# Optimization experiments

Measured on AMD Instinct MI355X. Metric: run time of the kernel, lower is better.

## Reference

```python
import jax, jax.numpy as jnp
import numpy as np

B, T, H = 1, 1024, 2048
HK, HV, DK, DV, K = 8, 16, 128, 128, 4
KD = HK * DK          # 1024
VD = HV * DV          # 2048
CD = 2 * KD + VD      # conv channels: q|k|v = 4096
EPS = 1e-6


def setup_inputs() -> dict:
    key = jax.random.key(0)
    ks = jax.random.split(key, 9)
    sc = lambda k, shape, s=0.02: jax.random.normal(k, shape, jnp.float32) * s
    return {
        "x": jax.random.normal(ks[0], (B, T, H), jnp.float32),
        "w_qkvz": sc(ks[1], (H, 2 * KD + 2 * VD)),
        "w_ba": sc(ks[2], (H, 2 * HV)),
        "conv_w": sc(ks[3], (CD, K), 0.2),
        "conv_b": jnp.zeros((CD,), jnp.float32),
        "a_log": jnp.log(jax.random.uniform(ks[4], (HV,), jnp.float32, 0.5, 4.0)),
        "dt_bias": sc(ks[5], (HV,), 0.5),
        "norm_w": jnp.ones((DV,), jnp.float32),
        "w_o": sc(ks[6], (VD, H)),
    }


def _l2norm(t):
    return t * jax.lax.rsqrt(jnp.sum(t * t, axis=-1, keepdims=True) + EPS)


def _gdn_forward(x, w_qkvz, w_ba, conv_w, conv_b, a_log, dt_bias, norm_w, w_o):
    # fused qkvz projection  [B,T, 2*KD + 2*VD]
    qkvz = x @ w_qkvz
    q, k, v, z = jnp.split(qkvz, [KD, 2 * KD, 2 * KD + VD], axis=-1)
    ba = x @ w_ba
    b, a = jnp.split(ba, [HV], axis=-1)  # [B,T,HV] each

    # causal depthwise conv1d over time on concatenated q|k|v channels, then SiLU
    mixed = jnp.concatenate([q, k, v], axis=-1)          # [B,T,CD]
    xc = jnp.moveaxis(mixed, 1, 2)                       # [B,CD,T]
    xc = jnp.pad(xc, ((0, 0), (0, 0), (K - 1, 0)))       # left pad -> causal
    yc = jax.lax.conv_general_dilated(
        xc, conv_w[:, None, :], (1,), "VALID",
        dimension_numbers=("NCH", "OIH", "NCH"), feature_group_count=CD)
    yc = jax.nn.silu(yc + conv_b[None, :, None])
    mixed = jnp.moveaxis(yc, 1, 2)                       # [B,T,CD]
    q, k, v = jnp.split(mixed, [KD, 2 * KD], axis=-1)

    q = q.reshape(B, T, HK, DK)
    k = k.reshape(B, T, HK, DK)
    v = v.reshape(B, T, HV, DV)

    # qk l2 norm (use_qk_l2norm_in_kernel) + GQA repeat + scale
    q = _l2norm(q)
    k = _l2norm(k)
    groups = HV // HK
    q = jnp.repeat(q, groups, axis=2)                    # [B,T,HV,DK]
    k = jnp.repeat(k, groups, axis=2)
    q = q * (DK ** -0.5)

    beta = jax.nn.sigmoid(b)                                        # [B,T,HV]
    g = -jnp.exp(a_log)[None, None, :] * jax.nn.softplus(a + dt_bias[None, None, :])

    # gated delta rule recurrence over time
    def step(S, inp):
        qt, kt, vt, gt, bt = inp                         # [B,HV,*]
        S = S * jnp.exp(gt)[..., None, None]             # decay
        pred = jnp.einsum("bhk,bhkv->bhv", kt, S)        # retrieve
        delta = (vt - pred) * bt[..., None]              # delta update
        S = S + kt[..., None] * delta[:, :, None, :]
        o = jnp.einsum("bhk,bhkv->bhv", qt, S)
        return S, o

    S0 = jnp.zeros((B, HV, DK, DV), jnp.float32)
    xs = tuple(jnp.moveaxis(t, 1, 0) for t in (q, k, v, g, beta))
    _, o = jax.lax.scan(step, S0, xs)                    # o: [T,B,HV,DV]
    o = jnp.moveaxis(o, 0, 1)                            # [B,T,HV,DV]

    # gated RMSNorm: gate first (silu), then normalize, then scale
    zg = z.reshape(B, T, HV, DV)
    h = o * jax.nn.silu(zg)
    h = h * jax.lax.rsqrt(jnp.mean(h * h, axis=-1, keepdims=True) + EPS)
    h = h * norm_w

    return h.reshape(B, T, VD) @ w_o                     # [B,T,H]


def reference(x, w_qkvz, w_ba, conv_w, conv_b, a_log, dt_bias, norm_w, w_o):
    return _gdn_forward(x, w_qkvz, w_ba, conv_w, conv_b, a_log, dt_bias, norm_w, w_o)
```

## Files before the change

### kernel.cpp

```cpp
#include <hip/hip_runtime.h>
#include <math.h>

typedef unsigned short u16;
using us4  = __attribute__((ext_vector_type(4))) unsigned short;
using us8  = __attribute__((ext_vector_type(8))) unsigned short;
using bf16x8 = __attribute__((ext_vector_type(8))) __bf16;
using f32x4v = __attribute__((ext_vector_type(4))) float;

#define T_    1024
#define H_    2048
#define HK_   8
#define HV_   16
#define KD_   1024
#define VD_   2048
#define CD_   4096
#define QN_   6144
#define NC_   16
#define C_    64

__device__ __forceinline__ u16 f2bf(float f) {
  unsigned u = __float_as_uint(f);
  u += 0x7fffu + ((u >> 16) & 1u);
  return (u16)(u >> 16);
}
__device__ __forceinline__ float bf2f(u16 h) {
  return __uint_as_float(((unsigned)h) << 16);
}
__device__ __forceinline__ int permk3(int r, int k) {
  return (k & ~63) | ((((k >> 3) & 7) ^ (r & 7)) << 3) | (k & 7);
}

__global__ void cast_bf16(const float* __restrict__ in, u16* __restrict__ out,
                          int n8) {
  int i = blockIdx.x * 256 + threadIdx.x;
  if (i >= n8) return;
  float4 a = ((const float4*)in)[i * 2];
  float4 b = ((const float4*)in)[i * 2 + 1];
  us8 r = {f2bf(a.x), f2bf(a.y), f2bf(a.z), f2bf(a.w),
           f2bf(b.x), f2bf(b.y), f2bf(b.z), f2bf(b.w)};
  const int row = i >> 8;
  const int ip = (i & ~7) | ((i & 7) ^ (row & 7));
  *(us8*)&out[(size_t)ip * 8] = r;
}

__global__ __launch_bounds__(256) void transpose_bf16(
    const float* __restrict__ in, u16* __restrict__ out, int R, int C) {
  __shared__ float tile[64][65];
  const int r0 = blockIdx.x * 64, c0 = blockIdx.y * 64;
  const int t = threadIdx.x;
  const int tr = t >> 4, tc4 = (t & 15) * 4;
#pragma unroll
  for (int i = 0; i < 4; ++i) {
    float4 v = *(const float4*)&in[(size_t)(r0 + tr + i * 16) * C + c0 + tc4];
    tile[tr + i * 16][tc4 + 0] = v.x;
    tile[tr + i * 16][tc4 + 1] = v.y;
    tile[tr + i * 16][tc4 + 2] = v.z;
    tile[tr + i * 16][tc4 + 3] = v.w;
  }
  __syncthreads();
#pragma unroll
  for (int i = 0; i < 4; ++i) {
    int oc = tr + i * 16;
    int row = c0 + oc;
    int k = r0 + tc4;
    us4 w = {f2bf(tile[tc4 + 0][oc]), f2bf(tile[tc4 + 1][oc]),
             f2bf(tile[tc4 + 2][oc]), f2bf(tile[tc4 + 3][oc])};
    *(us4*)&out[(size_t)row * R + permk3(row, k)] = w;
  }
}

__device__ __forceinline__ void gload_lds16(const void* g, void* l) {
  __builtin_amdgcn_global_load_lds(
      (const __attribute__((address_space(1))) void*)g,
      (__attribute__((address_space(3))) void*)l, 16, 0, 0);
}

__global__ __launch_bounds__(256) void gemm_bf16(
    const u16* __restrict__ A, const u16* __restrict__ Bt,
    float* __restrict__ Cq, int ldq, float* __restrict__ Cz, int ldz,
    int zsplit, int M, int N, int K) {
  __shared__ __align__(16) u16 As[2][8192];
  __shared__ __align__(16) u16 Bs[2][4096];
  const int tid  = threadIdx.x;
  const int wave = tid >> 6, lane = tid & 63;
  const int gy = N >> 6;
  const int ncolpx = gy >> 3;
  const int bid = blockIdx.x;
  const int xcd = bid & 7, idx = bid >> 3;
  const int row0 = (idx / ncolpx) * 128;
  const int col0 = (xcd * ncolpx + idx % ncolpx) * 64;
  const int wr = wave >> 1, wc = wave & 1;
  const int fr = lane & 15, fq = lane >> 4;

  const int sr8 = lane >> 3;
  const int sc8 = (lane & 7) * 8;
  const u16* gA = A  + (size_t)(row0 + wave * 32 + sr8) * K + sc8;
  const u16* gB = Bt + (size_t)(col0 + wave * 16 + sr8) * K + sc8;

  f32x4v acc[4][2] = {};
  const int nt = K >> 6;

  auto stage = [&](int p, int k0) {
#pragma unroll
    for (int j = 0; j < 4; ++j)
      gload_lds16(gA + (size_t)(j * 8) * K + k0,
                  &As[p][(wave * 32 + j * 8) * 64]);
#pragma unroll
    for (int j = 0; j < 2; ++j)
      gload_lds16(gB + (size_t)(j * 8) * K + k0,
                  &Bs[p][(wave * 16 + j * 8) * 64]);
  };

  stage(0, 0);
  asm volatile("s_waitcnt vmcnt(0)" ::: "memory");
  __syncthreads();

  int p = 0;
  for (int it = 0; it < nt; ++it) {
    if (it + 1 < nt) stage(p ^ 1, (it + 1) * 64);
#pragma unroll
    for (int kt = 0; kt < 2; ++kt) {
      bf16x8 af[4], bff[2];
#pragma unroll
      for (int mi = 0; mi < 4; ++mi) {
        const int r = wr * 64 + mi * 16 + fr;
        af[mi] = *(const bf16x8*)
            &As[p][r * 64 + kt * 32 + (((kt * 4 + fq) ^ (r & 7)) & 3) * 8
                   + ((((kt * 4 + fq) ^ (r & 7)) >> 2) - kt) * 32];
      }
#pragma unroll
      for (int ni = 0; ni < 2; ++ni) {
        const int r = wc * 32 + ni * 16 + fr;
        bff[ni] = *(const bf16x8*)
            &Bs[p][r * 64 + kt * 32 + (((kt * 4 + fq) ^ (r & 7)) & 3) * 8
                   + ((((kt * 4 + fq) ^ (r & 7)) >> 2) - kt) * 32];
      }
#pragma unroll
      for (int mi = 0; mi < 4; ++mi)
#pragma unroll
        for (int ni = 0; ni < 2; ++ni)
          acc[mi][ni] = __builtin_amdgcn_mfma_f32_16x16x32_bf16(
              af[mi], bff[ni], acc[mi][ni], 0, 0, 0);
    }
    if (it + 1 < nt) {
      asm volatile("s_waitcnt vmcnt(0)" ::: "memory");
      __syncthreads();
    }
    p ^= 1;
  }

  float* Cp; int ldc, cb;
  if (col0 < zsplit) { Cp = Cq; ldc = ldq; cb = col0; }
  else               { Cp = Cz; ldc = ldz; cb = col0 - zsplit; }
#pragma unroll
  for (int mi = 0; mi < 4; ++mi)
#pragma unroll
    for (int ni = 0; ni < 2; ++ni) {
      const int r  = row0 + wr * 64 + mi * 16 + fq * 4;
      const int cc = cb + wc * 32 + ni * 16 + fr;
#pragma unroll
      for (int j = 0; j < 4; ++j)
        Cp[(size_t)(r + j) * ldc + cc] = acc[mi][ni][j];
    }
}

__global__ __launch_bounds__(256) void ba_gbeta(
    const float* __restrict__ x, const float* __restrict__ w_ba,
    const float* __restrict__ a_log, const float* __restrict__ dt_bias,
    float* __restrict__ g, float* __restrict__ beta) {
  const int t = blockIdx.x;
  const int tid = threadIdx.x;
  __shared__ float xs[2048];
  __shared__ float red[8][32];
  {
    float4 v = *(const float4*)&x[(size_t)t * H_ + tid * 4];
    *(float4*)&xs[tid * 4] = v;
    float4 w = *(const float4*)&x[(size_t)t * H_ + 1024 + tid * 4];
    *(float4*)&xs[1024 + tid * 4] = w;
  }
  __syncthreads();
  const int c = tid & 31;
  const int chunk = tid >> 5;
  float p = 0.f;
  const int kb = chunk * 256;
#pragma unroll 4
  for (int k = kb; k < kb + 256; ++k) p = fmaf(xs[k], w_ba[k * 32 + c], p);
  red[chunk][c] = p;
  __syncthreads();
  if (tid < 32) {
    float s = 0.f;
#pragma unroll
    for (int i = 0; i < 8; ++i) s += red[i][c];
    if (c < 16) {
      beta[t * 16 + c] = 1.f / (1.f + expf(-s));
    } else {
      int h = c - 16;
      float xx = s + dt_bias[h];
      float sp = xx > 20.f ? xx : log1pf(expf(xx));
      g[t * 16 + h] = -expf(a_log[h]) * sp;
    }
  }
}

__global__ __launch_bounds__(512) void conv_silu_k(
    const float* __restrict__ qkvraw, const float* __restrict__ conv_w,
    const float* __restrict__ conv_b, float* __restrict__ qkvc,
    float* __restrict__ khat) {
  const int t = blockIdx.x;
  const int tid = threadIdx.x;
  const int c0 = tid * 8;
  float acc[8];
  float4 cb0 = *(const float4*)&conv_b[c0];
  float4 cb1 = *(const float4*)&conv_b[c0 + 4];
  acc[0] = cb0.x; acc[1] = cb0.y; acc[2] = cb0.z; acc[3] = cb0.w;
  acc[4] = cb1.x; acc[5] = cb1.y; acc[6] = cb1.z; acc[7] = cb1.w;
  float wv[8][4];
#pragma unroll
  for (int i = 0; i < 8; i += 2) {
    float4 w0 = *(const float4*)&conv_w[(c0 + i) * 4];
    float4 w1 = *(const float4*)&conv_w[(c0 + i + 1) * 4];
    wv[i][0] = w0.x; wv[i][1] = w0.y; wv[i][2] = w0.z; wv[i][3] = w0.w;
    wv[i+1][0] = w1.x; wv[i+1][1] = w1.y; wv[i+1][2] = w1.z; wv[i+1][3] = w1.w;
  }
#pragma unroll
  for (int j = 0; j < 4; ++j) {
    int tt = t - 3 + j;
    if (tt >= 0) {
      float4 a = *(const float4*)&qkvraw[(size_t)tt * CD_ + c0];
      float4 b = *(const float4*)&qkvraw[(size_t)tt * CD_ + c0 + 4];
      float xv[8] = {a.x, a.y, a.z, a.w, b.x, b.y, b.z, b.w};
#pragma unroll
      for (int i = 0; i < 8; ++i) acc[i] = fmaf(xv[i], wv[i][j], acc[i]);
    }
  }
  float y[8];
#pragma unroll
  for (int i = 0; i < 8; ++i) y[i] = acc[i] / (1.f + expf(-acc[i]));

  if (tid < 128 || tid >= 256) {
    float4 o0 = {y[0], y[1], y[2], y[3]};
    float4 o1 = {y[4], y[5], y[6], y[7]};
    *(float4*)&qkvc[(size_t)t * CD_ + c0]     = o0;
    *(float4*)&qkvc[(size_t)t * CD_ + c0 + 4] = o1;
  } else {
    float ss = 0.f;
#pragma unroll
    for (int i = 0; i < 8; ++i) ss = fmaf(y[i], y[i], ss);
#pragma unroll
    for (int off = 1; off < 16; off <<= 1) ss += __shfl_xor(ss, off);
    float rs = rsqrtf(ss + 1e-6f);
    const int head = (c0 - 1024) >> 7;
    const int d0 = (c0 - 1024) & 127;
    float4 o0 = {y[0] * rs, y[1] * rs, y[2] * rs, y[3] * rs};
    float4 o1 = {y[4] * rs, y[5] * rs, y[6] * rs, y[7] * rs};
    float* kout = &khat[((size_t)t * HK_ + head) * 128 + d0];
    *(float4*)&kout[0] = o0;
    *(float4*)&kout[4] = o1;
  }
}

#define SWZ(r) (((r) >> 2) & 7)

__device__ __forceinline__ float4 ldsw4(const float* base, int r, int dblk) {
  return *(const float4*)&base[r * 128 + ((dblk ^ SWZ(r)) << 2)];
}
__device__ __forceinline__ float ldsw1(const float* base, int r, int d) {
  return base[r * 128 + ((((d) >> 2) ^ SWZ(r)) << 2) + ((d) & 3)];
}

__global__ __launch_bounds__(512) void chunk_prep(
    const float* __restrict__ qkvc, const float* __restrict__ khat,
    const float* __restrict__ g, const float* __restrict__ beta,
    float* __restrict__ cgbuf, float* __restrict__ Wtg, float* __restrict__ Ug,
    float* __restrict__ Mqg, float* __restrict__ pQg) {
  const int c = blockIdx.x, hv = blockIdx.y, hk = hv >> 1;
  const int cid = c * 16 + hv;
  const int tid = threadIdx.x;
  __shared__ float Kl[8192], Ql[8192];
  __shared__ float AM[8320];
  __shared__ float cgl[64], bl[64], bp[64], rsl[64];
  float* At = AM;
  float* Mq = AM + 4160;

#pragma unroll
  for (int it = 0; it < 4; ++it) {
    int flat = it * 2048 + tid * 4;
    int row = flat >> 7, d = flat & 127;
    int pb = ((d >> 2) ^ SWZ(row)) << 2;
    int gt = c * 64 + row;
    float4 kv = *(const float4*)&khat[((size_t)gt * HK_ + hk) * 128 + d];
    float4 qv = *(const float4*)&qkvc[(size_t)gt * CD_ + hk * 128 + d];
    *(float4*)&Kl[row * 128 + pb] = kv;
    *(float4*)&Ql[row * 128 + pb] = qv;
  }
  if (tid < 64) {
    float s = g[(size_t)(c * 64 + tid) * HV_ + hv];
#pragma unroll
    for (int off = 1; off < 64; off <<= 1) {
      float t = __shfl_up(s, off);
      if (tid >= off) s += t;
    }
    cgl[tid] = s;
    cgbuf[cid * 64 + tid] = s;
    bl[tid] = beta[(size_t)(c * 64 + tid) * HV_ + hv];
  }
  __syncthreads();
  if (tid < 64) {
    float sq = 0.f;
#pragma unroll
    for (int dblk = 0; dblk < 32; ++dblk) {
      float4 q4 = ldsw4(Ql, tid, dblk);
      sq = fmaf(q4.x, q4.x, sq); sq = fmaf(q4.y, q4.y, sq);
      sq = fmaf(q4.z, q4.z, sq); sq = fmaf(q4.w, q4.w, sq);
    }
    rsl[tid] = rsqrtf(sq + 1e-6f) * 0.08838834764831845f;
    bp[tid] = bl[tid] * expf(cgl[tid]);
  }
  __syncthreads();

  const int i0 = (tid >> 5) * 4, j0 = (tid & 31) * 2;
  float kk[4][2], qk[4][2];
#pragma unroll
  for (int a = 0; a < 4; ++a)
#pragma unroll
    for (int b = 0; b < 2; ++b) { kk[a][b] = 0.f; qk[a][b] = 0.f; }
  for (int dblk = 0; dblk < 32; ++dblk) {
    float4 ka[4], qa[4], kb[2];
#pragma unroll
    for (int a = 0; a < 4; ++a) {
      ka[a] = ldsw4(Kl, i0 + a, dblk);
      qa[a] = ldsw4(Ql, i0 + a, dblk);
    }
#pragma unroll
    for (int b = 0; b < 2; ++b) kb[b] = ldsw4(Kl, j0 + b, dblk);
#pragma unroll
    for (int a = 0; a < 4; ++a)
#pragma unroll
      for (int b = 0; b < 2; ++b) {
        kk[a][b] = fmaf(ka[a].x, kb[b].x, kk[a][b]);
        kk[a][b] = fmaf(ka[a].y, kb[b].y, kk[a][b]);
        kk[a][b] = fmaf(ka[a].z, kb[b].z, kk[a][b]);
        kk[a][b] = fmaf(ka[a].w, kb[b].w, kk[a][b]);
        qk[a][b] = fmaf(qa[a].x, kb[b].x, qk[a][b]);
        qk[a][b] = fmaf(qa[a].y, kb[b].y, qk[a][b]);
        qk[a][b] = fmaf(qa[a].z, kb[b].z, qk[a][b]);
        qk[a][b] = fmaf(qa[a].w, kb[b].w, qk[a][b]);
      }
  }
#pragma unroll
  for (int a = 0; a < 4; ++a)
#pragma unroll
    for (int b = 0; b < 2; ++b) {
      int i = i0 + a, j = j0 + b;
      float e = expf(cgl[i] - cgl[j]);
      At[j * 65 + i] = (j < i) ? (-bl[i] * e * kk[a][b]) : 0.f;
      Mq[j * 65 + i] = (j <= i) ? (rsl[i] * e * qk[a][b]) : 0.f;
    }
  __syncthreads();

  float X[64];
  if (tid < 256) {
    if (tid < 128) {
#pragma unroll
      for (int j = 0; j < 64; ++j) X[j] = bp[j] * ldsw1(Kl, j, tid);
    } else {
      const int m = tid - 128;
#pragma unroll
      for (int j = 0; j < 64; ++j)
        X[j] = bl[j] * qkvc[(size_t)(c * 64 + j) * CD_ + 2 * KD_ + hv * 128 + m];
    }
#pragma unroll
    for (int j = 0; j < 63; ++j) {
      float xj = X[j];
#pragma unroll
      for (int i = j + 1; i < 64; ++i) X[i] = fmaf(At[j * 65 + i], xj, X[i]);
    }
    if (tid < 128) {
      size_t baseo = ((size_t)cid * 128 + tid) * 64;
#pragma unroll
      for (int j4 = 0; j4 < 16; ++j4) {
        float4 v = {X[j4 * 4], X[j4 * 4 + 1], X[j4 * 4 + 2], X[j4 * 4 + 3]};
        *(float4*)&Wtg[baseo + j4 * 4] = v;
      }
    }
  } else {
    const int t2 = tid - 256;
#pragma unroll
    for (int it = 0; it < 16; ++it) {
      int f = it * 256 + t2;
      int j = f >> 6, i = f & 63;
      Mqg[(size_t)cid * 4096 + f] = Mq[j * 65 + i];
    }
    const int i = t2 & 63;
    const float ei = expf(cgl[i]) * rsl[i];
#pragma unroll
    for (int it = 0; it < 32; ++it) {
      int d = it * 4 + (t2 >> 6);
      pQg[(size_t)cid * 8192 + d * 64 + i] = ei * ldsw1(Ql, i, d);
    }
  }
  __syncthreads();

  if (tid >= 128 && tid < 256) {
    const int m = tid - 128;
    float* Utr = AM;
#pragma unroll
    for (int j = 0; j < 64; ++j) Utr[j * 128 + m] = X[j];
  }
  __syncthreads();
  {
    const float* Utr = AM;
#pragma unroll
    for (int it = 0; it < 4; ++it) {
      int flat = it * 2048 + tid * 4;
      *(float4*)&Ug[(size_t)cid * 8192 + flat] = *(const float4*)&Utr[flat];
    }
  }
}

__global__ __launch_bounds__(512) void make_MBG(
    const float* __restrict__ Wtg, const float* __restrict__ pQg,
    const float* __restrict__ Ug, const float* __restrict__ Mqg,
    const float* __restrict__ khat, const float* __restrict__ cgbuf,
    u16* __restrict__ Mhi, u16* __restrict__ Mlo,
    float* __restrict__ Bg, float* __restrict__ Gtg) {
  const int c = blockIdx.x, hv = blockIdx.y, hk = hv >> 1;
  const int cid = c * 16 + hv;
  const int tid = threadIdx.x;
  __shared__ float Wl[64 * 128];
  __shared__ float Kel[64 * 128];
  __shared__ float Ul[64 * 128];
  __shared__ float Mql[64 * 64];
  const float cg63 = cgbuf[cid * 64 + 63];
  const float pC = expf(cg63);
#pragma unroll
  for (int it = 0; it < 4; ++it) {
    int f = it * 2048 + tid * 4;
    int d = f >> 6, j = f & 63;
    float4 w = *(const float4*)&Wtg[(size_t)cid * 8192 + f];
    Wl[(j + 0) * 128 + d] = w.x;
    Wl[(j + 1) * 128 + d] = w.y;
    Wl[(j + 2) * 128 + d] = w.z;
    Wl[(j + 3) * 128 + d] = w.w;
  }
#pragma unroll
  for (int it = 0; it < 4; ++it) {
    int f = it * 2048 + tid * 4;
    int j = f >> 7, d = f & 127;
    float esc = expf(cg63 - cgbuf[cid * 64 + j]);
    float4 kv = *(const float4*)&khat[((size_t)(c * 64 + j) * HK_ + hk) * 128 + d];
    float4 uv = *(const float4*)&Ug[(size_t)cid * 8192 + f];
    kv.x *= esc; kv.y *= esc; kv.z *= esc; kv.w *= esc;
    *(float4*)&Kel[f] = kv;
    *(float4*)&Ul[f] = uv;
  }
#pragma unroll
  for (int it = 0; it < 2; ++it) {
    int f = it * 2048 + tid * 4;
    *(float4*)&Mql[f] = *(const float4*)&Mqg[(size_t)cid * 4096 + f];
  }
  __syncthreads();

  const int d0 = (tid & 15) * 8, n0 = (tid >> 4) * 4;
  float ma[8][4] = {}, ba[8][4] = {};
  for (int j = 0; j < 64; ++j) {
    float4 k0 = *(const float4*)&Kel[j * 128 + d0];
    float4 k1 = *(const float4*)&Kel[j * 128 + d0 + 4];
    float4 w0 = *(const float4*)&Wl[j * 128 + n0];
    float4 u0 = *(const float4*)&Ul[j * 128 + n0];
    float ke[8] = {k0.x, k0.y, k0.z, k0.w, k1.x, k1.y, k1.z, k1.w};
    float wv[4] = {w0.x, w0.y, w0.z, w0.w};
    float uv[4] = {u0.x, u0.y, u0.z, u0.w};
#pragma unroll
    for (int a = 0; a < 8; ++a)
#pragma unroll
      for (int b = 0; b < 4; ++b) {
        ma[a][b] = fmaf(ke[a], wv[b], ma[a][b]);
        ba[a][b] = fmaf(ke[a], uv[b], ba[a][b]);
      }
  }
#pragma unroll
  for (int a = 0; a < 8; ++a) {
    const int d = d0 + a;
    us4 hi, lo;
#pragma unroll
    for (int b = 0; b < 4; ++b) {
      float m = ((d == n0 + b) ? pC : 0.f) - ma[a][b];
      u16 h = f2bf(m);
      hi[b] = h;
      lo[b] = f2bf(m - bf2f(h));
    }
    *(us4*)&Mhi[(size_t)cid * 16384 + d * 128 + n0] = hi;
    *(us4*)&Mlo[(size_t)cid * 16384 + d * 128 + n0] = lo;
    float4 b0 = {ba[a][0], ba[a][1], ba[a][2], ba[a][3]};
    *(float4*)&Bg[(size_t)cid * 16384 + d * 128 + n0] = b0;
  }

  const int dg = (tid & 31) * 4, ig = (tid >> 5) * 4;
  float ga[4][4] = {};
  for (int j = 0; j < 64; ++j) {
    float4 w4 = *(const float4*)&Wl[j * 128 + dg];
    float4 m0 = *(const float4*)&Mql[j * 64 + ig];
    float wv[4] = {w4.x, w4.y, w4.z, w4.w};
    float mv[4] = {m0.x, m0.y, m0.z, m0.w};
#pragma unroll
    for (int a = 0; a < 4; ++a)
#pragma unroll
      for (int b = 0; b < 4; ++b) ga[a][b] = fmaf(wv[a], mv[b], ga[a][b]);
  }
#pragma unroll
  for (int a = 0; a < 4; ++a) {
    const int d = dg + a;
    float4 p0 = *(const float4*)&pQg[(size_t)cid * 8192 + d * 64 + ig];
    float4 g0 = {p0.x - ga[a][0], p0.y - ga[a][1], p0.z - ga[a][2], p0.w - ga[a][3]};
    *(float4*)&Gtg[(size_t)cid * 8192 + d * 64 + ig] = g0;
  }
}

__global__ __launch_bounds__(512) void scan_S(
    const u16* __restrict__ Mhi, const u16* __restrict__ Mlo,
    const float* __restrict__ Bg, float* __restrict__ Sg) {
  const int flat = blockIdx.x;
  const int hv = (flat & 7) + 8 * (flat >> 6);
  const int vs = (flat >> 3) & 7;
  const int tid = threadIdx.x;
  const int wave = tid >> 6, lane = tid & 63;
  const int fr = lane & 15, fq = lane >> 4;
  const int wr = wave * 16;
  const int m0 = vs * 16;

  __shared__ u16 Sh[2][2048];
  __shared__ u16 Sl[2][2048];

  for (int i = tid; i < 2048; i += 512) { Sh[0][i] = 0; Sl[0][i] = 0; }
  {
    float* s0 = Sg + (size_t)hv * 16384 + m0;
#pragma unroll
    for (int it = 0; it < 4; ++it) {
      int idx = it * 512 + tid;
      s0[(size_t)(idx >> 4) * 128 + (idx & 15)] = 0.f;
    }
  }
  __syncthreads();

  bf16x8 MhA[4], MlA[4], MhB[4], MlB[4];
  float bvA[4], bvB[4];
  {
    const u16* Mh0 = Mhi + (size_t)hv * 16384;
    const u16* Ml0 = Mlo + (size_t)hv * 16384;
#pragma unroll
    for (int kt = 0; kt < 4; ++kt) {
      size_t off = (size_t)(wr + fr) * 128 + kt * 32 + fq * 8;
      MhA[kt] = *(const bf16x8*)&Mh0[off];
      MlA[kt] = *(const bf16x8*)&Ml0[off];
    }
    const float* Bc = Bg + (size_t)hv * 16384 + m0;
#pragma unroll
    for (int j = 0; j < 4; ++j)
      bvA[j] = Bc[(size_t)(wr + fq * 4 + j) * 128 + fr];
  }
  int p = 0;

  auto step = [&](int c, bf16x8 (&MhC)[4], bf16x8 (&MlC)[4], float (&bvC)[4],
                  bf16x8 (&MhN)[4], bf16x8 (&MlN)[4], float (&bvN)[4]) {
    if (c + 1 < NC_ - 1) {
      const u16* MhP = Mhi + (size_t)((c + 1) * 16 + hv) * 16384;
      const u16* MlP = Mlo + (size_t)((c + 1) * 16 + hv) * 16384;
#pragma unroll
      for (int kt = 0; kt < 4; ++kt) {
        size_t off = (size_t)(wr + fr) * 128 + kt * 32 + fq * 8;
        MhN[kt] = *(const bf16x8*)&MhP[off];
        MlN[kt] = *(const bf16x8*)&MlP[off];
      }
      const float* BcN = Bg + (size_t)((c + 1) * 16 + hv) * 16384 + m0;
#pragma unroll
      for (int j = 0; j < 4; ++j)
        bvN[j] = BcN[(size_t)(wr + fq * 4 + j) * 128 + fr];
    }

    f32x4v acc = {};
#pragma unroll
    for (int kt = 0; kt < 4; ++kt) {
      const int m = fr;
      const int byte = m * 256 + ((kt * 64 + fq * 16) ^ ((m & 7) << 4));
      bf16x8 BhF = *(const bf16x8*)((const char*)&Sh[p][0] + byte);
      bf16x8 BlF = *(const bf16x8*)((const char*)&Sl[p][0] + byte);
      acc = __builtin_amdgcn_mfma_f32_16x16x32_bf16(MlC[kt], BhF, acc, 0, 0, 0);
      acc = __builtin_amdgcn_mfma_f32_16x16x32_bf16(MhC[kt], BlF, acc, 0, 0, 0);
      acc = __builtin_amdgcn_mfma_f32_16x16x32_bf16(MhC[kt], BhF, acc, 0, 0, 0);
    }

    float* Sn = Sg + (size_t)((c + 1) * 16 + hv) * 16384 + m0;
    const int k0 = wr + fq * 4;
    const int m = fr;
    us4 h4, l4;
#pragma unroll
    for (int j = 0; j < 4; ++j) {
      float v = acc[j] + bvC[j];
      Sn[(size_t)(k0 + j) * 128 + m] = v;
      u16 h = f2bf(v);
      h4[j] = h;
      l4[j] = f2bf(v - bf2f(h));
    }
    const int wbyte = m * 256 + ((k0 * 2) ^ ((m & 7) << 4));
    *(us4*)((char*)&Sh[p ^ 1][0] + wbyte) = h4;
    *(us4*)((char*)&Sl[p ^ 1][0] + wbyte) = l4;
    __syncthreads();
    p ^= 1;
  };

  for (int cc = 0; cc < NC_ - 1; cc += 2) {
    step(cc, MhA, MlA, bvA, MhB, MlB, bvB);
    if (cc + 1 < NC_ - 1) step(cc + 1, MhB, MlB, bvB, MhA, MlA, bvA);
  }
}

__global__ __launch_bounds__(256) void chunk_out(
    const float* __restrict__ Mqg, const float* __restrict__ Ug,
    const float* __restrict__ Gtg, const float* __restrict__ Sg,
    float* __restrict__ o) {
  const int c = blockIdx.x, hv = blockIdx.y;
  const int cid = c * 16 + hv;
  const int tid = threadIdx.x;
  __shared__ float Mql[64 * 64];
  __shared__ float Ul[64 * 128];
  __shared__ float Gtl[128 * 64];
  __shared__ float Sl[128 * 128];
#pragma unroll
  for (int it = 0; it < 4; ++it) {
    int f = it * 1024 + tid * 4;
    *(float4*)&Mql[f] = *(const float4*)&Mqg[(size_t)cid * 4096 + f];
  }
#pragma unroll
  for (int it = 0; it < 8; ++it) {
    int f = it * 1024 + tid * 4;
    *(float4*)&Ul[f]  = *(const float4*)&Ug[(size_t)cid * 8192 + f];
    *(float4*)&Gtl[f] = *(const float4*)&Gtg[(size_t)cid * 8192 + f];
  }
#pragma unroll
  for (int it = 0; it < 16; ++it) {
    int f = it * 1024 + tid * 4;
    *(float4*)&Sl[f] = *(const float4*)&Sg[(size_t)cid * 16384 + f];
  }
  __syncthreads();

  const int i0 = (tid & 15) * 4, m0 = (tid >> 4) * 8;
  float oa[4][8] = {};
  for (int j = 0; j < 64; ++j) {
    float4 mq = *(const float4*)&Mql[j * 64 + i0];
    float4 u0 = *(const float4*)&Ul[j * 128 + m0];
    float4 u1 = *(const float4*)&Ul[j * 128 + m0 + 4];
    float mv[4] = {mq.x, mq.y, mq.z, mq.w};
    float uv[8] = {u0.x, u0.y, u0.z, u0.w, u1.x, u1.y, u1.z, u1.w};
#pragma unroll
    for (int a = 0; a < 4; ++a)
#pragma unroll
      for (int b = 0; b < 8; ++b) oa[a][b] = fmaf(mv[a], uv[b], oa[a][b]);
  }
  for (int d = 0; d < 128; ++d) {
    float4 gt = *(const float4*)&Gtl[d * 64 + i0];
    float4 s0 = *(const float4*)&Sl[d * 128 + m0];
    float4 s1 = *(const float4*)&Sl[d * 128 + m0 + 4];
    float gv[4] = {gt.x, gt.y, gt.z, gt.w};
    float sv[8] = {s0.x, s0.y, s0.z, s0.w, s1.x, s1.y, s1.z, s1.w};
#pragma unroll
    for (int a = 0; a < 4; ++a)
#pragma unroll
      for (int b = 0; b < 8; ++b) oa[a][b] = fmaf(gv[a], sv[b], oa[a][b]);
  }
#pragma unroll
  for (int a = 0; a < 4; ++a) {
    const int t = c * 64 + i0 + a;
    float4 o0 = {oa[a][0], oa[a][1], oa[a][2], oa[a][3]};
    float4 o1 = {oa[a][4], oa[a][5], oa[a][6], oa[a][7]};
    *(float4*)&o[((size_t)t * HV_ + hv) * 128 + m0]     = o0;
    *(float4*)&o[((size_t)t * HV_ + hv) * 128 + m0 + 4] = o1;
  }
}

__global__ void gated_rmsnorm(const float* __restrict__ o,
                              const float* __restrict__ zbuf,
                              const float* __restrict__ norm_w,
                              u16* __restrict__ h) {
  const int t = blockIdx.x, hv = blockIdx.y, d = threadIdx.x;
  float ov = o[((size_t)t * HV_ + hv) * 128 + d];
  float zv = zbuf[(size_t)t * VD_ + hv * 128 + d];
  float hc = ov * (zv / (1.f + expf(-zv)));
  float ss = hc * hc;
#pragma unroll
  for (int off = 32; off >= 1; off >>= 1) ss += __shfl_xor(ss, off);
  __shared__ float s2[2];
  if ((d & 63) == 0) s2[d >> 6] = ss;
  __syncthreads();
  float tot = s2[0] + s2[1];
  float r = rsqrtf(tot * (1.f / 128.f) + 1e-6f);
  const int k = hv * 128 + d;
  h[(size_t)t * VD_ + permk3(t, k)] = f2bf(hc * r * norm_w[d]);
}

extern "C" void kernel_launch(void* const* d_in, const int* in_sizes, int n_in,
                              void* d_out, int out_size, void* d_ws, size_t ws_size,
                              hipStream_t stream) {
  const float* x       = (const float*)d_in[0];
  const float* w_qkvz  = (const float*)d_in[1];
  const float* w_ba    = (const float*)d_in[2];
  const float* conv_w  = (const float*)d_in[3];
  const float* conv_b  = (const float*)d_in[4];
  const float* a_log   = (const float*)d_in[5];
  const float* dt_bias = (const float*)d_in[6];
  const float* norm_w  = (const float*)d_in[7];
  const float* w_o     = (const float*)d_in[8];
  float* out = (float*)d_out;

  float* ws = (float*)d_ws;
  float* qkvraw = ws;
  float* zbuf   = ws + 4194304;
  float* qkvc   = ws + 6291456;
  float* khat   = ws + 10485760;
  float* gbuf   = ws + 11534336;
  float* bbuf   = ws + 11550720;
  float* cgbuf  = ws + 11567104;
  float* obuf   = ws + 11583488;
  float* Wtg    = ws + 13680640;
  float* pQg    = ws + 15777792;
  float* Ug     = ws + 17874944;
  float* Mqg    = ws + 19972096;
  float* Gtg    = ws + 21020672;

  u16* xb   = (u16*)obuf;
  u16* wqt  = (u16*)Wtg;
  u16* Mhi  = (u16*)qkvc;
  u16* Mlo  = (u16*)(qkvc + 2097152);
  float* Bg = qkvraw;
  float* Sg = Wtg;
  u16* wot  = (u16*)qkvc;
  u16* hb   = (u16*)khat;

  cast_bf16<<<1024, 256, 0, stream>>>(x, xb, 262144);
  transpose_bf16<<<dim3(32, 96), 256, 0, stream>>>(w_qkvz, wqt, H_, QN_);
  gemm_bf16<<<768, 256, 0, stream>>>(xb, wqt, qkvraw, CD_, zbuf, VD_,
                                     CD_, T_, QN_, H_);
  ba_gbeta<<<T_, 256, 0, stream>>>(x, w_ba, a_log, dt_bias, gbuf, bbuf);
  conv_silu_k<<<T_, 512, 0, stream>>>(qkvraw, conv_w, conv_b, qkvc, khat);
  chunk_prep<<<dim3(NC_, HV_), 512, 0, stream>>>(
      qkvc, khat, gbuf, bbuf, cgbuf, Wtg, Ug, Mqg, pQg);
  make_MBG<<<dim3(NC_, HV_), 512, 0, stream>>>(
      Wtg, pQg, Ug, Mqg, khat, cgbuf, Mhi, Mlo, Bg, Gtg);
  scan_S<<<128, 512, 0, stream>>>(Mhi, Mlo, Bg, Sg);
  transpose_bf16<<<dim3(32, 32), 256, 0, stream>>>(w_o, wot, VD_, H_);
  chunk_out<<<dim3(NC_, HV_), 256, 0, stream>>>(Mqg, Ug, Gtg, Sg, obuf);
  gated_rmsnorm<<<dim3(T_, HV_), 128, 0, stream>>>(obuf, zbuf, norm_w, hb);
  gemm_bf16<<<256, 256, 0, stream>>>(hb, wot, out, VD_, out, VD_,
                                     VD_, T_, VD_, H_);
}
```

Before: 246.7 us.

## Compute chunk KK^T and QK^T with split-bf16 MFMA, vectorize triangular solve

The chunk_prep kernel now stores K and Q in shared memory as hi/lo bf16 pairs with an XOR swizzle. It computes the 64x64 K·K^T and Q·K^T products with three-term split-bf16 MFMA instructions instead of scalar FP32 FMAs. The At matrix stride is padded to 68 so the forward-substitution loop can read coefficients as float4. Shared memory use grows and the split-bf16 path is slightly less exact than FP32, but the work is moved onto matrix cores.

```diff
diff --git a/kernel.cpp b/kernel.cpp
--- a/kernel.cpp
+++ b/kernel.cpp
@@ -261,9 +261,6 @@
 
 #define SWZ(r) (((r) >> 2) & 7)
 
-__device__ __forceinline__ float4 ldsw4(const float* base, int r, int dblk) {
-  return *(const float4*)&base[r * 128 + ((dblk ^ SWZ(r)) << 2)];
-}
 __device__ __forceinline__ float ldsw1(const float* base, int r, int d) {
   return base[r * 128 + ((((d) >> 2) ^ SWZ(r)) << 2) + ((d) & 3)];
 }
@@ -276,22 +273,34 @@
   const int c = blockIdx.x, hv = blockIdx.y, hk = hv >> 1;
   const int cid = c * 16 + hv;
   const int tid = threadIdx.x;
-  __shared__ float Kl[8192], Ql[8192];
-  __shared__ float AM[8320];
+  __shared__ __align__(16) float Kl[8192];
+  __shared__ __align__(16) u16 KhiL[8192], KloL[8192];
+  __shared__ __align__(16) u16 QhiL[8192], QloL[8192];
+  __shared__ __align__(16) float AM[8512];
   __shared__ float cgl[64], bl[64], bp[64], rsl[64];
   float* At = AM;
-  float* Mq = AM + 4160;
+  float* Mq = AM + 4352;
 
 #pragma unroll
   for (int it = 0; it < 4; ++it) {
     int flat = it * 2048 + tid * 4;
     int row = flat >> 7, d = flat & 127;
-    int pb = ((d >> 2) ^ SWZ(row)) << 2;
     int gt = c * 64 + row;
     float4 kv = *(const float4*)&khat[((size_t)gt * HK_ + hk) * 128 + d];
     float4 qv = *(const float4*)&qkvc[(size_t)gt * CD_ + hk * 128 + d];
+    int pb = ((d >> 2) ^ SWZ(row)) << 2;
     *(float4*)&Kl[row * 128 + pb] = kv;
-    *(float4*)&Ql[row * 128 + pb] = qv;
+    int ba = row * 128 + (((d >> 3) ^ (row & 15)) << 3) + (d & 7);
+    us4 kh = {f2bf(kv.x), f2bf(kv.y), f2bf(kv.z), f2bf(kv.w)};
+    us4 kl = {f2bf(kv.x - bf2f(kh[0])), f2bf(kv.y - bf2f(kh[1])),
+              f2bf(kv.z - bf2f(kh[2])), f2bf(kv.w - bf2f(kh[3]))};
+    us4 qh = {f2bf(qv.x), f2bf(qv.y), f2bf(qv.z), f2bf(qv.w)};
+    us4 ql = {f2bf(qv.x - bf2f(qh[0])), f2bf(qv.y - bf2f(qh[1])),
+              f2bf(qv.z - bf2f(qh[2])), f2bf(qv.w - bf2f(qh[3]))};
+    *(us4*)&KhiL[ba] = kh;
+    *(us4*)&KloL[ba] = kl;
+    *(us4*)&QhiL[ba] = qh;
+    *(us4*)&QloL[ba] = ql;
   }
   if (tid < 64) {
     float s = g[(size_t)(c * 64 + tid) * HV_ + hv];
@@ -308,54 +317,63 @@
   if (tid < 64) {
     float sq = 0.f;
 #pragma unroll
-    for (int dblk = 0; dblk < 32; ++dblk) {
-      float4 q4 = ldsw4(Ql, tid, dblk);
-      sq = fmaf(q4.x, q4.x, sq); sq = fmaf(q4.y, q4.y, sq);
-      sq = fmaf(q4.z, q4.z, sq); sq = fmaf(q4.w, q4.w, sq);
+    for (int ch = 0; ch < 16; ++ch) {
+      int ba = tid * 128 + ((ch ^ (tid & 15)) << 3);
+      us8 h8 = *(const us8*)&QhiL[ba];
+      us8 l8 = *(const us8*)&QloL[ba];
+#pragma unroll
+      for (int e = 0; e < 8; ++e) {
+        float q = bf2f(h8[e]) + bf2f(l8[e]);
+        sq = fmaf(q, q, sq);
+      }
     }
     rsl[tid] = rsqrtf(sq + 1e-6f) * 0.08838834764831845f;
     bp[tid] = bl[tid] * expf(cgl[tid]);
   }
   __syncthreads();
 
-  const int i0 = (tid >> 5) * 4, j0 = (tid & 31) * 2;
-  float kk[4][2], qk[4][2];
-#pragma unroll
-  for (int a = 0; a < 4; ++a)
-#pragma unroll
-    for (int b = 0; b < 2; ++b) { kk[a][b] = 0.f; qk[a][b] = 0.f; }
-  for (int dblk = 0; dblk < 32; ++dblk) {
-    float4 ka[4], qa[4], kb[2];
-#pragma unroll
-    for (int a = 0; a < 4; ++a) {
-      ka[a] = ldsw4(Kl, i0 + a, dblk);
-      qa[a] = ldsw4(Ql, i0 + a, dblk);
-    }
-#pragma unroll
-    for (int b = 0; b < 2; ++b) kb[b] = ldsw4(Kl, j0 + b, dblk);
-#pragma unroll
-    for (int a = 0; a < 4; ++a)
-#pragma unroll
-      for (int b = 0; b < 2; ++b) {
-        kk[a][b] = fmaf(ka[a].x, kb[b].x, kk[a][b]);
-        kk[a][b] = fmaf(ka[a].y, kb[b].y, kk[a][b]);
-        kk[a][b] = fmaf(ka[a].z, kb[b].z, kk[a][b]);
-        kk[a][b] = fmaf(ka[a].w, kb[b].w, kk[a][b]);
-        qk[a][b] = fmaf(qa[a].x, kb[b].x, qk[a][b]);
-        qk[a][b] = fmaf(qa[a].y, kb[b].y, qk[a][b]);
-        qk[a][b] = fmaf(qa[a].z, kb[b].z, qk[a][b]);
-        qk[a][b] = fmaf(qa[a].w, kb[b].w, qk[a][b]);
-      }
-  }
-#pragma unroll
-  for (int a = 0; a < 4; ++a)
-#pragma unroll
-    for (int b = 0; b < 2; ++b) {
-      int i = i0 + a, j = j0 + b;
-      float e = expf(cgl[i] - cgl[j]);
-      At[j * 65 + i] = (j < i) ? (-bl[i] * e * kk[a][b]) : 0.f;
-      Mq[j * 65 + i] = (j <= i) ? (rsl[i] * e * qk[a][b]) : 0.f;
-    }
+  {
+    const int wv = tid >> 6, lane = tid & 63;
+    const int fr = lane & 15, fq = lane >> 4;
+    const int ib = wv & 3;
+    const int jb0 = (wv >> 2) * 2;
+    const int ra = ib * 16 + fr;
+    bf16x8 KhA[4], KlA[4], QhA[4], QlA[4];
+#pragma unroll
+    for (int ks = 0; ks < 4; ++ks) {
+      int ca = ra * 128 + (((ks * 4 + fq) ^ fr) << 3);
+      KhA[ks] = *(const bf16x8*)&KhiL[ca];
+      KlA[ks] = *(const bf16x8*)&KloL[ca];
+      QhA[ks] = *(const bf16x8*)&QhiL[ca];
+      QlA[ks] = *(const bf16x8*)&QloL[ca];
+    }
+#pragma unroll
+    for (int u = 0; u < 2; ++u) {
+      const int jb = jb0 + u;
+      const int rb = jb * 16 + fr;
+      f32x4v ak = {}, aq = {};
+#pragma unroll
+      for (int ks = 0; ks < 4; ++ks) {
+        int cb = rb * 128 + (((ks * 4 + fq) ^ fr) << 3);
+        bf16x8 Bh = *(const bf16x8*)&KhiL[cb];
+        bf16x8 Bl = *(const bf16x8*)&KloL[cb];
+        ak = __builtin_amdgcn_mfma_f32_16x16x32_bf16(KlA[ks], Bh, ak, 0, 0, 0);
+        ak = __builtin_amdgcn_mfma_f32_16x16x32_bf16(KhA[ks], Bl, ak, 0, 0, 0);
+        ak = __builtin_amdgcn_mfma_f32_16x16x32_bf16(KhA[ks], Bh, ak, 0, 0, 0);
+        aq = __builtin_amdgcn_mfma_f32_16x16x32_bf16(QlA[ks], Bh, aq, 0, 0, 0);
+        aq = __builtin_amdgcn_mfma_f32_16x16x32_bf16(QhA[ks], Bl, aq, 0, 0, 0);
+        aq = __builtin_amdgcn_mfma_f32_16x16x32_bf16(QhA[ks], Bh, aq, 0, 0, 0);
+      }
+#pragma unroll
+      for (int reg = 0; reg < 4; ++reg) {
+        const int i = ib * 16 + fq * 4 + reg;
+        const int j = jb * 16 + fr;
+        float e = expf(cgl[i] - cgl[j]);
+        At[j * 68 + i] = (j < i) ? (-bl[i] * e * ak[reg]) : 0.f;
+        Mq[j * 65 + i] = (j <= i) ? (rsl[i] * e * aq[reg]) : 0.f;
+      }
+    }
+  }
   __syncthreads();
 
   float X[64];
@@ -370,10 +388,23 @@
         X[j] = bl[j] * qkvc[(size_t)(c * 64 + j) * CD_ + 2 * KD_ + hv * 128 + m];
     }
 #pragma unroll
-    for (int j = 0; j < 63; ++j) {
-      float xj = X[j];
-#pragma unroll
-      for (int i = j + 1; i < 64; ++i) X[i] = fmaf(At[j * 65 + i], xj, X[i]);
+    for (int jb4 = 0; jb4 < 16; ++jb4) {
+#pragma unroll
+      for (int jj = 0; jj < 4; ++jj) {
+        const int j = jb4 * 4 + jj;
+        float xj = X[j];
+#pragma unroll
+        for (int ii = jj + 1; ii < 4; ++ii)
+          X[jb4 * 4 + ii] = fmaf(At[j * 68 + jb4 * 4 + ii], xj, X[jb4 * 4 + ii]);
+#pragma unroll
+        for (int gg = jb4 + 1; gg < 16; ++gg) {
+          float4 a4 = *(const float4*)&At[j * 68 + gg * 4];
+          X[gg * 4 + 0] = fmaf(a4.x, xj, X[gg * 4 + 0]);
+          X[gg * 4 + 1] = fmaf(a4.y, xj, X[gg * 4 + 1]);
+          X[gg * 4 + 2] = fmaf(a4.z, xj, X[gg * 4 + 2]);
+          X[gg * 4 + 3] = fmaf(a4.w, xj, X[gg * 4 + 3]);
+        }
+      }
     }
     if (tid < 128) {
       size_t baseo = ((size_t)cid * 128 + tid) * 64;
@@ -396,7 +427,9 @@
 #pragma unroll
     for (int it = 0; it < 32; ++it) {
       int d = it * 4 + (t2 >> 6);
-      pQg[(size_t)cid * 8192 + d * 64 + i] = ei * ldsw1(Ql, i, d);
+      int ba = i * 128 + (((d >> 3) ^ (i & 15)) << 3) + (d & 7);
+      float q = bf2f(QhiL[ba]) + bf2f(QloL[ba]);
+      pQg[(size_t)cid * 8192 + d * 64 + i] = ei * q;
     }
   }
   __syncthreads();
```

Result: slower. 348.2 us (+41.1%).
